# Optimization experiments

Measured on AMD Instinct MI355X. Metric: run time of the kernel, lower is better.

## Reference

```python
import jax, jax.numpy as jnp
import numpy as np

K_NEIGS = 3
M_PROB = 1.0
EPS = 1e-12


def _gen_G_single(ft):
    """Build normalized hypergraph Laplacian G [N,N] from node coords ft [N,3].

    Mirrors construct_H_with_KNN (is_probH=True, m_prob=1) + generate_G_from_H
    from the HGNN reference code: per-center KNN hyperedges with probabilistic
    incidence exp(-d^2/(m_prob*avg_d)^2), then G = Dv^-1/2 H De^-1 H^T Dv^-1/2.
    """
    N = ft.shape[0]
    # squared pairwise Euclidean distances [N,N]
    sq_norm = jnp.sum(ft * ft, axis=1)
    sq = jnp.maximum(sq_norm[:, None] + sq_norm[None, :] - 2.0 * ft @ ft.T, 0.0)
    dist = jnp.sqrt(sq + EPS)
    avg_dis = jnp.mean(dist, axis=1)  # per-center mean distance [N]
    # K nearest neighbors per center (self is always included: sq[c,c]=0)
    neg_sq, idx = jax.lax.top_k(-sq, K_NEIGS)  # [N,K]
    # prob incidence: exp(-d^2 / (m_prob*avg)^2); neg_sq = -d^2
    vals = jnp.exp(neg_sq / (M_PROB * avg_dis[:, None]) ** 2)  # [N,K]
    # H[node, edge]: column c holds the K neighbors of center c
    H = jnp.zeros((N, N), ft.dtype).at[idx, jnp.arange(N)[:, None]].set(vals)
    de = jnp.sum(H, axis=0)              # edge degrees [N]
    dv = jnp.sum(H, axis=1)              # vertex degrees [N]
    inv_de = 1.0 / de
    dv2 = dv ** -0.5
    HW = H * inv_de[None, :]
    G = (dv2[:, None] * (HW @ H.T)) * dv2[None, :]
    return G


def reference(x, W1, b1, Wc, bc):
    # gen_G: per-batch hypergraph G [B,N,N]
    G = jax.vmap(_gen_G_single)(x)
    # HGNN_conv with both args = G: out = G @ (G @ W1 + b1)  -> [B,N,H1]
    f = jnp.matmul(G, jnp.matmul(G, W1) + b1)
    # max-pool over nodes, then classifier
    f = jnp.max(f, axis=1)               # [B,H1]
    return f @ Wc + bc                   # [B,class_num]


def setup_inputs() -> dict:
    key = jax.random.key(0)
    k1, k2, k3, k4, k5 = jax.random.split(key, 5)
    B, N, H1, C = 4, 2048, 128, 8
    x = jax.random.normal(k1, (B, N, 3), dtype=jnp.float32)
    W1 = jax.random.normal(k2, (N, H1), dtype=jnp.float32) / np.sqrt(N)
    b1 = jax.random.normal(k3, (H1,), dtype=jnp.float32) * 0.01
    Wc = jax.random.normal(k4, (H1, C), dtype=jnp.float32) / np.sqrt(H1)
    bc = jax.random.normal(k5, (C,), dtype=jnp.float32) * 0.01
    return {"x": x, "W1": W1, "b1": b1, "Wc": Wc, "bc": bc}
```

## Files before the change

kernel.cpp:

```cpp
#include <hip/hip_runtime.h>
#include <math.h>

#define NN 2048
#define BB 4
#define HD 128
#define CNUM 8
#define WPB 4
#define CAP 64
#define NPB 8
#define NCH (NN / NPB)

typedef unsigned long long u64;

__device__ __forceinline__ u64 pack_key(float sq, int j) {
    return ((u64)__float_as_uint(sq) << 32) | (unsigned)j;
}
__device__ __forceinline__ void ins3(u64 k, u64& k0, u64& k1, u64& k2) {
    u64 a = k  < k2 ? k  : k2;
    u64 b = k0 > a  ? k0 : a;
    k0    = k0 < a  ? k0 : a;
    k2    = k1 > b  ? k1 : b;
    k1    = k1 < b  ? k1 : b;
}

__global__ __launch_bounds__(256) void k_dist(
        const float* __restrict__ x,
        int* __restrict__ idx, float* __restrict__ vals,
        float* __restrict__ de, float* __restrict__ dv,
        int* __restrict__ cnt, int2* __restrict__ rev) {
    __shared__ float4 sp[NN];
    const int b = blockIdx.y;
    const float* xb = x + (size_t)b * NN * 3;
    for (int q = threadIdx.x; q < NN; q += 256) {
        const float a = xb[3 * q], c = xb[3 * q + 1], d = xb[3 * q + 2];
        sp[q] = make_float4(a, c, d, a * a + c * c + d * d);
    }
    __syncthreads();

    const int wave = threadIdx.x >> 6;
    const int lane = threadIdx.x & 63;
    const int i = blockIdx.x * WPB + wave;
    const float4 ci = sp[i];
    u64 k0 = ~0ull, k1 = ~0ull, k2 = ~0ull;
    float dsA = 0.f, dsB = 0.f;
    for (int t = lane; t < NN; t += 256) {
        const float4 pa = sp[t];
        const float4 pv = sp[t + 64];
        const float4 pc = sp[t + 128];
        const float4 pd = sp[t + 192];
        const float qa = fmaxf(ci.w + pa.w - 2.0f * (ci.x * pa.x + ci.y * pa.y + ci.z * pa.z), 0.0f);
        const float qb = fmaxf(ci.w + pv.w - 2.0f * (ci.x * pv.x + ci.y * pv.y + ci.z * pv.z), 0.0f);
        const float qc = fmaxf(ci.w + pc.w - 2.0f * (ci.x * pc.x + ci.y * pc.y + ci.z * pc.z), 0.0f);
        const float qd = fmaxf(ci.w + pd.w - 2.0f * (ci.x * pd.x + ci.y * pd.y + ci.z * pd.z), 0.0f);
        dsA += __builtin_amdgcn_sqrtf(qa + 1e-12f) + __builtin_amdgcn_sqrtf(qc + 1e-12f);
        dsB += __builtin_amdgcn_sqrtf(qb + 1e-12f) + __builtin_amdgcn_sqrtf(qd + 1e-12f);
        ins3(pack_key(qa, t),       k0, k1, k2);
        ins3(pack_key(qb, t + 64),  k0, k1, k2);
        ins3(pack_key(qc, t + 128), k0, k1, k2);
        ins3(pack_key(qd, t + 192), k0, k1, k2);
    }
    float dsum = dsA + dsB;
    for (int off = 32; off > 0; off >>= 1) {
        const u64 o0 = __shfl_xor(k0, off);
        const u64 o1 = __shfl_xor(k1, off);
        const u64 o2 = __shfl_xor(k2, off);
        dsum += __shfl_xor(dsum, off);
        ins3(o0, k0, k1, k2);
        ins3(o1, k0, k1, k2);
        ins3(o2, k0, k1, k2);
    }
    if (lane == 0) {
        const float s0 = __uint_as_float((unsigned)(k0 >> 32));
        const float s1 = __uint_as_float((unsigned)(k1 >> 32));
        const float s2 = __uint_as_float((unsigned)(k2 >> 32));
        const int   i0 = (int)(k0 & 0xffffffffu);
        const int   i1 = (int)(k1 & 0xffffffffu);
        const int   i2 = (int)(k2 & 0xffffffffu);
        const float avg = dsum * (1.0f / NN);
        const float inva2 = 1.0f / (avg * avg);
        const float v0 = expf(-s0 * inva2);
        const float v1 = expf(-s1 * inva2);
        const float v2 = expf(-s2 * inva2);
        const int base = (b * NN + i) * 3;
        idx[base] = i0; idx[base + 1] = i1; idx[base + 2] = i2;
        vals[base] = v0; vals[base + 1] = v1; vals[base + 2] = v2;
        de[b * NN + i] = v0 + v1 + v2;
        atomicAdd(&dv[b * NN + i0], v0);
        atomicAdd(&dv[b * NN + i1], v1);
        atomicAdd(&dv[b * NN + i2], v2);
        const int p0 = atomicAdd(&cnt[b * NN + i0], 1);
        if (p0 < CAP) rev[((size_t)(b * NN + i0)) * CAP + p0] = make_int2(i, __float_as_int(v0));
        const int p1 = atomicAdd(&cnt[b * NN + i1], 1);
        if (p1 < CAP) rev[((size_t)(b * NN + i1)) * CAP + p1] = make_int2(i, __float_as_int(v1));
        const int p2 = atomicAdd(&cnt[b * NN + i2], 1);
        if (p2 < CAP) rev[((size_t)(b * NN + i2)) * CAP + p2] = make_int2(i, __float_as_int(v2));
    }
}

__global__ __launch_bounds__(256) void k_conv1(
        const float* __restrict__ W1, const float* __restrict__ b1,
        const int* __restrict__ idx, const float* __restrict__ vals,
        const float* __restrict__ de, const float* __restrict__ dv,
        const int* __restrict__ cnt, const int2* __restrict__ rev,
        float* __restrict__ f1) {
    const int b = blockIdx.y;
    const int i = blockIdx.x * 2 + (threadIdx.x >> 7);
    const int h = threadIdx.x & (HD - 1);
    const int ni = b * NN + i;
    const int cn = min(cnt[ni], CAP);
    float acc = 0.f;
    for (int s = 0; s < cn; ++s) {
        const int2 r = rev[(size_t)ni * CAP + s];
        const int e = r.x;
        const float v = __int_as_float(r.y);
        const int eb = (b * NN + e) * 3;
        const int j0 = idx[eb], j1 = idx[eb + 1], j2 = idx[eb + 2];
        const float v0 = vals[eb], v1 = vals[eb + 1], v2 = vals[eb + 2];
        const float ide = 1.0f / de[b * NN + e];
        const float g0 = v0 * rsqrtf(dv[b * NN + j0]);
        const float g1 = v1 * rsqrtf(dv[b * NN + j1]);
        const float g2 = v2 * rsqrtf(dv[b * NN + j2]);
        const float y = ide * (g0 * W1[j0 * HD + h] + g1 * W1[j1 * HD + h] + g2 * W1[j2 * HD + h]);
        acc += v * y;
    }
    f1[(size_t)ni * HD + h] = rsqrtf(dv[ni]) * acc + b1[h];
}

__global__ __launch_bounds__(256) void k_conv2(
        const int* __restrict__ idx, const float* __restrict__ vals,
        const float* __restrict__ de, const float* __restrict__ dv,
        const int* __restrict__ cnt, const int2* __restrict__ rev,
        const float* __restrict__ f1, float* __restrict__ pmax) {
    __shared__ float smx[2][HD];
    const int b = blockIdx.y;
    const int sub = threadIdx.x >> 7;
    const int h = threadIdx.x & (HD - 1);
    float mx = -INFINITY;
    for (int t = 0; t < NPB / 2; ++t) {
        const int i = blockIdx.x * NPB + t * 2 + sub;
        const int ni = b * NN + i;
        const int cn = min(cnt[ni], CAP);
        float acc = 0.f;
        for (int s = 0; s < cn; ++s) {
            const int2 r = rev[(size_t)ni * CAP + s];
            const int e = r.x;
            const float v = __int_as_float(r.y);
            const int eb = (b * NN + e) * 3;
            const int j0 = idx[eb], j1 = idx[eb + 1], j2 = idx[eb + 2];
            const float v0 = vals[eb], v1 = vals[eb + 1], v2 = vals[eb + 2];
            const float ide = 1.0f / de[b * NN + e];
            const float g0 = v0 * rsqrtf(dv[b * NN + j0]);
            const float g1 = v1 * rsqrtf(dv[b * NN + j1]);
            const float g2 = v2 * rsqrtf(dv[b * NN + j2]);
            const float y = ide * (g0 * f1[((size_t)(b * NN + j0)) * HD + h]
                                 + g1 * f1[((size_t)(b * NN + j1)) * HD + h]
                                 + g2 * f1[((size_t)(b * NN + j2)) * HD + h]);
            acc += v * y;
        }
        mx = fmaxf(mx, rsqrtf(dv[ni]) * acc);
    }
    smx[sub][h] = mx;
    __syncthreads();
    if (sub == 0)
        pmax[((size_t)b * NCH + blockIdx.x) * HD + h] = fmaxf(smx[0][h], smx[1][h]);
}

__global__ void k_pool2(const float* __restrict__ Wc, const float* __restrict__ bc,
                        const float* __restrict__ pmax, float* __restrict__ out) {
    __shared__ float s2[2][HD];
    const int b = blockIdx.x;
    const int h = threadIdx.x & (HD - 1);
    const int half = threadIdx.x >> 7;
    float mx = -INFINITY;
    for (int c = half; c < NCH; c += 2)
        mx = fmaxf(mx, pmax[((size_t)b * NCH + c) * HD + h]);
    s2[half][h] = mx;
    __syncthreads();
    if (half == 0) s2[0][h] = fmaxf(s2[0][h], s2[1][h]);
    __syncthreads();
    if (threadIdx.x < CNUM) {
        float acc = bc[threadIdx.x];
        for (int q = 0; q < HD; ++q) acc += s2[0][q] * Wc[q * CNUM + threadIdx.x];
        out[b * CNUM + threadIdx.x] = acc;
    }
}

extern "C" void kernel_launch(void* const* d_in, const int* in_sizes, int n_in,
                              void* d_out, int out_size, void* d_ws, size_t ws_size,
                              hipStream_t stream) {
    const float* x  = (const float*)d_in[0];
    const float* W1 = (const float*)d_in[1];
    const float* b1 = (const float*)d_in[2];
    const float* Wc = (const float*)d_in[3];
    const float* bc = (const float*)d_in[4];
    float* out = (float*)d_out;

    float* ws = (float*)d_ws;
    float* dv   = ws;
    int*   cnt  = (int*)(dv + BB * NN);
    float* de   = (float*)(cnt + BB * NN);
    int*   idx  = (int*)(de + BB * NN);
    float* vals = (float*)(idx + BB * NN * 3);
    int2*  rev  = (int2*)(vals + BB * NN * 3);
    float* f1   = (float*)(rev + (size_t)BB * NN * CAP);
    float* pmax = f1 + (size_t)BB * NN * HD;

    hipMemsetAsync(dv, 0, (size_t)2 * BB * NN * sizeof(float), stream);

    k_dist <<<dim3(NN / WPB, BB), 256, 0, stream>>>(x, idx, vals, de, dv, cnt, rev);
    k_conv1<<<dim3(NN / 2,  BB), 256, 0, stream>>>(W1, b1, idx, vals, de, dv, cnt, rev, f1);
    k_conv2<<<dim3(NN / NPB, BB), 256, 0, stream>>>(idx, vals, de, dv, cnt, rev, f1, pmax);
    k_pool2<<<BB, 256, 0, stream>>>(Wc, bc, pmax, out);
}
```

Measured before the change: 139.8 us.

## Precompute sparse G row lists, stream points from global, fuse max-pool via atomics

Adds a k_gbuild pass that expands each node's reverse hyperedge list into a flat (neighbor, weight) list for one row of G. The conv kernels then do a single gather-FMA per entry instead of recomputing idx/vals/de/dv normalizations twice. k_dist now reads precomputed float4 points from global memory instead of filling a 32KB shared array in every block. Max-pooling uses an order-preserving uint atomicMax, which removes the separate pool kernel. In exchange there are two extra small launches, and any row with more than CAPG entries is silently truncated.

```diff
diff --git a/kernel.cpp b/kernel.cpp
--- a/kernel.cpp
+++ b/kernel.cpp
@@ -7,8 +7,8 @@
 #define CNUM 8
 #define WPB 4
 #define CAP 64
-#define NPB 8
-#define NCH (NN / NPB)
+#define CAPG 128
+#define NPB 4
 
 typedef unsigned long long u64;
 
@@ -23,31 +23,30 @@
     k1    = k1 < b  ? k1 : b;
 }
 
+__global__ void k_prep(const float* __restrict__ x, float4* __restrict__ pts) {
+    const int t = blockIdx.x * 256 + threadIdx.x;
+    const float a = x[3 * t], c = x[3 * t + 1], d = x[3 * t + 2];
+    pts[t] = make_float4(a, c, d, a * a + c * c + d * d);
+}
+
 __global__ __launch_bounds__(256) void k_dist(
-        const float* __restrict__ x,
+        const float4* __restrict__ pts,
         int* __restrict__ idx, float* __restrict__ vals,
         float* __restrict__ de, float* __restrict__ dv,
         int* __restrict__ cnt, int2* __restrict__ rev) {
-    __shared__ float4 sp[NN];
-    const int b = blockIdx.y;
-    const float* xb = x + (size_t)b * NN * 3;
-    for (int q = threadIdx.x; q < NN; q += 256) {
-        const float a = xb[3 * q], c = xb[3 * q + 1], d = xb[3 * q + 2];
-        sp[q] = make_float4(a, c, d, a * a + c * c + d * d);
-    }
-    __syncthreads();
-
+    const int b = blockIdx.y;
+    const float4* pb = pts + b * NN;
     const int wave = threadIdx.x >> 6;
     const int lane = threadIdx.x & 63;
     const int i = blockIdx.x * WPB + wave;
-    const float4 ci = sp[i];
+    const float4 ci = pb[i];
     u64 k0 = ~0ull, k1 = ~0ull, k2 = ~0ull;
     float dsA = 0.f, dsB = 0.f;
     for (int t = lane; t < NN; t += 256) {
-        const float4 pa = sp[t];
-        const float4 pv = sp[t + 64];
-        const float4 pc = sp[t + 128];
-        const float4 pd = sp[t + 192];
+        const float4 pa = pb[t];
+        const float4 pv = pb[t + 64];
+        const float4 pc = pb[t + 128];
+        const float4 pd = pb[t + 192];
         const float qa = fmaxf(ci.w + pa.w - 2.0f * (ci.x * pa.x + ci.y * pa.y + ci.z * pa.z), 0.0f);
         const float qb = fmaxf(ci.w + pv.w - 2.0f * (ci.x * pv.x + ci.y * pv.y + ci.z * pv.z), 0.0f);
         const float qc = fmaxf(ci.w + pc.w - 2.0f * (ci.x * pc.x + ci.y * pc.y + ci.z * pc.z), 0.0f);
@@ -97,40 +96,55 @@
     }
 }
 
+__global__ void k_gbuild(const int* __restrict__ idx, const float* __restrict__ vals,
+                         const float* __restrict__ de, const float* __restrict__ dv,
+                         const int* __restrict__ cnt, const int2* __restrict__ rev,
+                         int2* __restrict__ glist, int* __restrict__ gn) {
+    const int b = blockIdx.y;
+    const int i = blockIdx.x * 256 + threadIdx.x;
+    const int ni = b * NN + i;
+    const int cn = min(cnt[ni], CAP);
+    const float wi = rsqrtf(dv[ni]);
+    int m = 0;
+    for (int s = 0; s < cn; ++s) {
+        const int2 r = rev[(size_t)ni * CAP + s];
+        const int e = r.x;
+        const float coef = wi * __int_as_float(r.y) / de[b * NN + e];
+        const int eb = (b * NN + e) * 3;
+        #pragma unroll
+        for (int t = 0; t < 3; ++t) {
+            const int j = idx[eb + t];
+            const float gv = coef * vals[eb + t] * rsqrtf(dv[b * NN + j]);
+            if (m < CAPG) glist[(size_t)ni * CAPG + m] = make_int2(j, __float_as_int(gv));
+            ++m;
+        }
+    }
+    gn[ni] = min(m, CAPG);
+}
+
 __global__ __launch_bounds__(256) void k_conv1(
         const float* __restrict__ W1, const float* __restrict__ b1,
-        const int* __restrict__ idx, const float* __restrict__ vals,
-        const float* __restrict__ de, const float* __restrict__ dv,
-        const int* __restrict__ cnt, const int2* __restrict__ rev,
+        const int2* __restrict__ glist, const int* __restrict__ gn,
         float* __restrict__ f1) {
     const int b = blockIdx.y;
     const int i = blockIdx.x * 2 + (threadIdx.x >> 7);
     const int h = threadIdx.x & (HD - 1);
     const int ni = b * NN + i;
-    const int cn = min(cnt[ni], CAP);
-    float acc = 0.f;
-    for (int s = 0; s < cn; ++s) {
-        const int2 r = rev[(size_t)ni * CAP + s];
-        const int e = r.x;
-        const float v = __int_as_float(r.y);
-        const int eb = (b * NN + e) * 3;
-        const int j0 = idx[eb], j1 = idx[eb + 1], j2 = idx[eb + 2];
-        const float v0 = vals[eb], v1 = vals[eb + 1], v2 = vals[eb + 2];
-        const float ide = 1.0f / de[b * NN + e];
-        const float g0 = v0 * rsqrtf(dv[b * NN + j0]);
-        const float g1 = v1 * rsqrtf(dv[b * NN + j1]);
-        const float g2 = v2 * rsqrtf(dv[b * NN + j2]);
-        const float y = ide * (g0 * W1[j0 * HD + h] + g1 * W1[j1 * HD + h] + g2 * W1[j2 * HD + h]);
-        acc += v * y;
-    }
-    f1[(size_t)ni * HD + h] = rsqrtf(dv[ni]) * acc + b1[h];
+    const int n = gn[ni];
+    const int2* gl = glist + (size_t)ni * CAPG;
+    float acc = b1[h];
+    int2 cur = gl[0];
+    for (int s = 0; s < n; ++s) {
+        const int2 nxt = gl[min(s + 1, n - 1)];
+        acc += __int_as_float(cur.y) * W1[cur.x * HD + h];
+        cur = nxt;
+    }
+    f1[(size_t)ni * HD + h] = acc;
 }
 
 __global__ __launch_bounds__(256) void k_conv2(
-        const int* __restrict__ idx, const float* __restrict__ vals,
-        const float* __restrict__ de, const float* __restrict__ dv,
-        const int* __restrict__ cnt, const int2* __restrict__ rev,
-        const float* __restrict__ f1, float* __restrict__ pmax) {
+        const int2* __restrict__ glist, const int* __restrict__ gn,
+        const float* __restrict__ f1, unsigned* __restrict__ pmaxK) {
     __shared__ float smx[2][HD];
     const int b = blockIdx.y;
     const int sub = threadIdx.x >> 7;
@@ -139,49 +153,39 @@
     for (int t = 0; t < NPB / 2; ++t) {
         const int i = blockIdx.x * NPB + t * 2 + sub;
         const int ni = b * NN + i;
-        const int cn = min(cnt[ni], CAP);
+        const int n = gn[ni];
+        const int2* gl = glist + (size_t)ni * CAPG;
         float acc = 0.f;
-        for (int s = 0; s < cn; ++s) {
-            const int2 r = rev[(size_t)ni * CAP + s];
-            const int e = r.x;
-            const float v = __int_as_float(r.y);
-            const int eb = (b * NN + e) * 3;
-            const int j0 = idx[eb], j1 = idx[eb + 1], j2 = idx[eb + 2];
-            const float v0 = vals[eb], v1 = vals[eb + 1], v2 = vals[eb + 2];
-            const float ide = 1.0f / de[b * NN + e];
-            const float g0 = v0 * rsqrtf(dv[b * NN + j0]);
-            const float g1 = v1 * rsqrtf(dv[b * NN + j1]);
-            const float g2 = v2 * rsqrtf(dv[b * NN + j2]);
-            const float y = ide * (g0 * f1[((size_t)(b * NN + j0)) * HD + h]
-                                 + g1 * f1[((size_t)(b * NN + j1)) * HD + h]
-                                 + g2 * f1[((size_t)(b * NN + j2)) * HD + h]);
-            acc += v * y;
+        int2 cur = gl[0];
+        for (int s = 0; s < n; ++s) {
+            const int2 nxt = gl[min(s + 1, n - 1)];
+            acc += __int_as_float(cur.y) * f1[((size_t)(b * NN + cur.x)) * HD + h];
+            cur = nxt;
         }
-        mx = fmaxf(mx, rsqrtf(dv[ni]) * acc);
+        mx = fmaxf(mx, acc);
     }
     smx[sub][h] = mx;
     __syncthreads();
-    if (sub == 0)
-        pmax[((size_t)b * NCH + blockIdx.x) * HD + h] = fmaxf(smx[0][h], smx[1][h]);
-}
-
-__global__ void k_pool2(const float* __restrict__ Wc, const float* __restrict__ bc,
-                        const float* __restrict__ pmax, float* __restrict__ out) {
-    __shared__ float s2[2][HD];
-    const int b = blockIdx.x;
-    const int h = threadIdx.x & (HD - 1);
-    const int half = threadIdx.x >> 7;
-    float mx = -INFINITY;
-    for (int c = half; c < NCH; c += 2)
-        mx = fmaxf(mx, pmax[((size_t)b * NCH + c) * HD + h]);
-    s2[half][h] = mx;
+    if (sub == 0) {
+        const float v = fmaxf(smx[0][h], smx[1][h]);
+        unsigned u = __float_as_uint(v);
+        u = (u & 0x80000000u) ? ~u : (u | 0x80000000u);
+        atomicMax(&pmaxK[b * HD + h], u);
+    }
+}
+
+__global__ void k_cls(const float* __restrict__ Wc, const float* __restrict__ bc,
+                      const unsigned* __restrict__ pmaxK, float* __restrict__ out) {
+    __shared__ float smax[HD];
+    const int b = blockIdx.x, h = threadIdx.x;
+    unsigned u = pmaxK[b * HD + h];
+    u = (u & 0x80000000u) ? (u ^ 0x80000000u) : ~u;
+    smax[h] = __uint_as_float(u);
     __syncthreads();
-    if (half == 0) s2[0][h] = fmaxf(s2[0][h], s2[1][h]);
-    __syncthreads();
-    if (threadIdx.x < CNUM) {
-        float acc = bc[threadIdx.x];
-        for (int q = 0; q < HD; ++q) acc += s2[0][q] * Wc[q * CNUM + threadIdx.x];
-        out[b * CNUM + threadIdx.x] = acc;
+    if (h < CNUM) {
+        float acc = bc[h];
+        for (int q = 0; q < HD; ++q) acc += smax[q] * Wc[q * CNUM + h];
+        out[b * CNUM + h] = acc;
     }
 }
 
@@ -195,20 +199,24 @@
     const float* bc = (const float*)d_in[4];
     float* out = (float*)d_out;
 
-    float* ws = (float*)d_ws;
-    float* dv   = ws;
-    int*   cnt  = (int*)(dv + BB * NN);
-    float* de   = (float*)(cnt + BB * NN);
-    int*   idx  = (int*)(de + BB * NN);
-    float* vals = (float*)(idx + BB * NN * 3);
-    int2*  rev  = (int2*)(vals + BB * NN * 3);
-    float* f1   = (float*)(rev + (size_t)BB * NN * CAP);
-    float* pmax = f1 + (size_t)BB * NN * HD;
-
-    hipMemsetAsync(dv, 0, (size_t)2 * BB * NN * sizeof(float), stream);
-
-    k_dist <<<dim3(NN / WPB, BB), 256, 0, stream>>>(x, idx, vals, de, dv, cnt, rev);
-    k_conv1<<<dim3(NN / 2,  BB), 256, 0, stream>>>(W1, b1, idx, vals, de, dv, cnt, rev, f1);
-    k_conv2<<<dim3(NN / NPB, BB), 256, 0, stream>>>(idx, vals, de, dv, cnt, rev, f1, pmax);
-    k_pool2<<<BB, 256, 0, stream>>>(Wc, bc, pmax, out);
-}
+    float4*   pts   = (float4*)d_ws;
+    float*    dv    = (float*)(pts + BB * NN);
+    int*      cnt   = (int*)(dv + BB * NN);
+    unsigned* pmaxK = (unsigned*)(cnt + BB * NN);
+    float*    de    = (float*)(pmaxK + BB * HD);
+    int*      idx   = (int*)(de + BB * NN);
+    float*    vals  = (float*)(idx + BB * NN * 3);
+    int*      gn    = (int*)(vals + BB * NN * 3);
+    int2*     rev   = (int2*)(gn + BB * NN);
+    int2*     glist = rev + (size_t)BB * NN * CAP;
+    float*    f1    = (float*)(glist + (size_t)BB * NN * CAPG);
+
+    hipMemsetAsync(dv, 0, (size_t)(2 * BB * NN + BB * HD) * sizeof(float), stream);
+
+    k_prep  <<<BB * NN / 256, 256, 0, stream>>>(x, pts);
+    k_dist  <<<dim3(NN / WPB, BB), 256, 0, stream>>>(pts, idx, vals, de, dv, cnt, rev);
+    k_gbuild<<<dim3(NN / 256, BB), 256, 0, stream>>>(idx, vals, de, dv, cnt, rev, glist, gn);
+    k_conv1 <<<dim3(NN / 2, BB), 256, 0, stream>>>(W1, b1, glist, gn, f1);
+    k_conv2 <<<dim3(NN / NPB, BB), 256, 0, stream>>>(glist, gn, f1, pmaxK);
+    k_cls   <<<BB, HD, 0, stream>>>(Wc, bc, pmaxK, out);
+}
```

Measured after the change: 139.4 us. Within noise of the previous version (-0.3%).
